# Kernel tuning notes

Measured on AMD Instinct MI355X. Metric: run time of the kernel, lower is better.

The kernel has to match this reference:

```python
import jax, jax.numpy as jnp
import numpy as np

B, S, D, H = 2, 2048, 1024, 16
DH = D // H
EPS = 1e-5
LAMBDA_INIT = 0.8


def setup_inputs() -> dict:
    key = jax.random.key(0)
    ks = jax.random.split(key, 16)
    w_std = 1.0 / np.sqrt(D)
    lam_std = LAMBDA_INIT / np.sqrt(DH)
    return {
        "x": jax.random.normal(ks[0], (B, S, D), jnp.float32),
        # Linear weights stored [in, out] (y = x @ W + b), equivalent to torch W.T
        "Wq": jax.random.normal(ks[1], (D, D), jnp.float32) * w_std,
        "bq": jax.random.normal(ks[2], (D,), jnp.float32) * 0.02,
        "Wk": jax.random.normal(ks[3], (D, D), jnp.float32) * w_std,
        "bk": jax.random.normal(ks[4], (D,), jnp.float32) * 0.02,
        "Wv": jax.random.normal(ks[5], (D, D), jnp.float32) * w_std,
        "bv": jax.random.normal(ks[6], (D,), jnp.float32) * 0.02,
        "Wo": jax.random.normal(ks[7], (D, D), jnp.float32) * w_std,
        "bo": jax.random.normal(ks[8], (D,), jnp.float32) * 0.02,
        "lq1": jax.random.normal(ks[9], (H, DH), jnp.float32) * lam_std,
        "lk1": jax.random.normal(ks[10], (H, DH), jnp.float32) * lam_std,
        "lq2": jax.random.normal(ks[11], (H, DH), jnp.float32) * lam_std,
        "lk2": jax.random.normal(ks[12], (H, DH), jnp.float32) * lam_std,
        # per-head GroupNorm(1, head_dim) affine params (torch default init)
        "gn_w": jnp.ones((H, DH), jnp.float32),
        "gn_b": jnp.zeros((H, DH), jnp.float32),
    }


def reference(x, Wq, bq, Wk, bk, Wv, bv, Wo, bo, lq1, lk1, lq2, lk2, gn_w, gn_b):
    b, s, d = x.shape
    h, dh = lq1.shape
    scale = dh ** -0.5

    q = (x @ Wq + bq).reshape(b, s, h, dh)
    k = (x @ Wk + bk).reshape(b, s, h, dh)
    v = (x @ Wv + bv).reshape(b, s, h, dh)

    # differential lambda per head: exp(<lq1,lk1>) - exp(<lq2,lk2>) + lambda_init
    lam = jnp.exp((lq1 * lk1).sum(-1)) - jnp.exp((lq2 * lk2).sum(-1)) + LAMBDA_INIT  # [H]

    scores = jnp.einsum("bihd,bjhd->bhij", q, k) * scale * lam[None, :, None, None]
    attn = jax.nn.softmax(scores, axis=-1)  # no mask in default call path
    out = jnp.einsum("bhij,bjhd->bihd", attn, v)  # [B,S,H,DH]

    # per-head GroupNorm(1, head_dim): normalize over (seq, head_dim) per (batch, head)
    mean = out.mean(axis=(1, 3), keepdims=True)
    var = out.var(axis=(1, 3), keepdims=True)
    normed = (out - mean) * jax.lax.rsqrt(var + EPS)
    normed = normed * gn_w[None, None, :, :] + gn_b[None, None, :, :]

    y = normed.reshape(b, s, d) @ Wo + bo
    return y
```

## Files before the change

kernel.cpp:

```cpp
#include <hip/hip_runtime.h>

#define S_LEN 2048
#define D_DIM 1024
#define H_NUM 16
#define DH 64
#define EPS_GN 1e-5f
#define LAMBDA_INIT 0.8f

typedef unsigned short bfu;
typedef __attribute__((ext_vector_type(8))) short bf16x8;
typedef __attribute__((ext_vector_type(4))) float f32x4;

union FragU { uint4 u; bf16x8 f; };

__device__ inline float bf2f(bfu u){
  union { unsigned int i; float f; } c; c.i = ((unsigned int)u) << 16; return c.f;
}
__device__ inline bfu f2bf(float f){
  union { float f; unsigned int u; } c; c.f = f;
  unsigned int r = c.u + 0x7fffu + ((c.u >> 16) & 1u);
  return (bfu)(r >> 16);
}
__device__ inline unsigned cvtpk(float lo, float hi){
  unsigned r;
  asm("v_cvt_pk_bf16_f32 %0, %1, %2" : "=v"(r) : "v"(lo), "v"(hi));
  return r;
}
__device__ inline void gload16(const void* g, void* lds){
  __builtin_amdgcn_global_load_lds(
      (const __attribute__((address_space(1))) void*)g,
      (__attribute__((address_space(3))) void*)lds, 16, 0, 0);
}
__device__ inline float ldx(const void* p, size_t i, int isf32){
  return isf32 ? ((const float*)p)[i] : bf2f(((const bfu*)p)[i]);
}
__device__ inline float wave_sum(float x){
  #pragma unroll
  for (int off = 32; off; off >>= 1) x += __shfl_xor(x, off, 64);
  return x;
}

__global__ void lambda_kernel(const void* __restrict__ lq1, const void* __restrict__ lk1,
                              const void* __restrict__ lq2, const void* __restrict__ lk2,
                              const unsigned int* __restrict__ gnw_bits,
                              int* __restrict__ flag, float* __restrict__ lam,
                              float* __restrict__ sums){
  const int isf32 = (gnw_bits[0] == 0x3F800000u) ? 1 : 0;
  int t = threadIdx.x;
  if (t == 0) flag[0] = isf32;
  sums[t] = 0.f;
  if (t < H_NUM){
    float s1 = 0.f, s2 = 0.f;
    for (int d = 0; d < DH; ++d){
      s1 += ldx(lq1, t*DH+d, isf32) * ldx(lk1, t*DH+d, isf32);
      s2 += ldx(lq2, t*DH+d, isf32) * ldx(lk2, t*DH+d, isf32);
    }
    lam[t] = expf(s1) - expf(s2) + LAMBDA_INIT;
  }
}

__global__ __launch_bounds__(256) void prep_all(
    const void* __restrict__ x,
    const void* __restrict__ w0, const void* __restrict__ w1,
    const void* __restrict__ w2, const void* __restrict__ w3,
    const int* __restrict__ flag, bfu* __restrict__ xb, bfu* __restrict__ wt)
{
  const int isf32 = flag[0];
  if (blockIdx.x < 2048){
    size_t i = ((size_t)blockIdx.x * 256 + threadIdx.x) * 8;
    if (isf32){
      const float* xf = (const float*)x;
      float4 a = *(const float4*)(xf + i);
      float4 b = *(const float4*)(xf + i + 4);
      bfu o[8] = {f2bf(a.x),f2bf(a.y),f2bf(a.z),f2bf(a.w),f2bf(b.x),f2bf(b.y),f2bf(b.z),f2bf(b.w)};
      *(uint4*)(xb + i) = *(const uint4*)o;
    } else {
      *(uint4*)(xb + i) = *(const uint4*)((const bfu*)x + i);
    }
    return;
  }
  const int widx = blockIdx.x - 2048;
  const int wsel = widx >> 8, tile = widx & 255;
  const void* W = (wsel==0)?w0:(wsel==1)?w1:(wsel==2)?w2:w3;
  bfu* dst = wt + (size_t)wsel * D_DIM * D_DIM;
  __shared__ float Ts[64][65];
  const int r0 = (tile >> 4) * 64, c0 = (tile & 15) * 64;
  const int ty = threadIdx.x >> 6, tx = threadIdx.x & 63;
  #pragma unroll
  for (int rr = 0; rr < 16; ++rr){
    int row = ty*16 + rr;
    Ts[row][tx] = ldx(W, (size_t)(r0 + row) * D_DIM + c0 + tx, isf32);
  }
  __syncthreads();
  #pragma unroll
  for (int rr = 0; rr < 2; ++rr){
    const int row = rr*32 + (threadIdx.x >> 3);
    const int txg = (threadIdx.x & 7) * 8;
    bfu outv[8];
    #pragma unroll
    for (int k2 = 0; k2 < 8; ++k2) outv[k2] = f2bf(Ts[txg + k2][row]);
    *(uint4*)(dst + (size_t)(c0 + row) * D_DIM + r0 + txg) = *(const uint4*)outv;
  }
}

__global__ __launch_bounds__(256, 3) void qkv_mfma(
    const bfu* __restrict__ xb, const bfu* __restrict__ wt,
    const void* __restrict__ bq, const void* __restrict__ bk, const void* __restrict__ bv,
    const float* __restrict__ lam, const int* __restrict__ flag,
    bfu* __restrict__ qb, bfu* __restrict__ kb, bfu* __restrict__ vt)
{
  const int isf32 = flag[0];
  const int z = blockIdx.z;
  const bfu* Wt = wt + (size_t)z * D_DIM * D_DIM;
  const void* bias = (z==0)?bq:(z==1)?bk:bv;

  __shared__ __align__(16) ushort As[2][128][32];
  __shared__ __align__(16) ushort Bs[2][128][32];
  const int m0 = blockIdx.x * 128, n0 = blockIdx.y * 128;
  const int t = threadIdx.x, w = t >> 6, lane = t & 63;
  const int quad = lane >> 4, l15 = lane & 15;
  const int mbase = (w >> 1) * 64, nbase = (w & 1) * 64;

  const int srow = w*32 + (lane >> 2);
  const int gchunk = (lane & 3) ^ ((lane >> 3) & 3);
  const size_t aoff = (size_t)(m0 + srow) * D_DIM + gchunk*8;
  const size_t boff = (size_t)(n0 + srow) * D_DIM + gchunk*8;

#define STAGE(buf, k0) {                                                  \
    gload16(xb + aoff + (k0),            &As[buf][w*32][0]);              \
    gload16(xb + aoff + 16*D_DIM + (k0), &As[buf][w*32+16][0]);           \
    gload16(Wt + boff + (k0),            &Bs[buf][w*32][0]);              \
    gload16(Wt + boff + 16*D_DIM + (k0), &Bs[buf][w*32+16][0]);           \
  }

  f32x4 acc[4][4];
  #pragma unroll
  for (int i = 0; i < 4; ++i)
    #pragma unroll
    for (int j = 0; j < 4; ++j){ f32x4 zz = {0.f,0.f,0.f,0.f}; acc[i][j] = zz; }

  const int chq = (quad ^ ((l15 >> 1) & 3)) * 8;

  STAGE(0, 0)
  int buf = 0;
  for (int k0 = 0; k0 < D_DIM; k0 += 32){
    if (k0 + 32 < D_DIM){
      STAGE(buf ^ 1, k0 + 32)
      asm volatile("s_waitcnt vmcnt(4)" ::: "memory");
    } else {
      asm volatile("s_waitcnt vmcnt(0)" ::: "memory");
    }
    __builtin_amdgcn_s_barrier();
    FragU af[4], bf[4];
    #pragma unroll
    for (int mt = 0; mt < 4; ++mt) af[mt].u = *(const uint4*)&As[buf][mbase + mt*16 + l15][chq];
    #pragma unroll
    for (int nt = 0; nt < 4; ++nt) bf[nt].u = *(const uint4*)&Bs[buf][nbase + nt*16 + l15][chq];
    #pragma unroll
    for (int mt = 0; mt < 4; ++mt)
      #pragma unroll
      for (int nt = 0; nt < 4; ++nt)
        acc[mt][nt] = __builtin_amdgcn_mfma_f32_16x16x32_bf16(af[mt].f, bf[nt].f, acc[mt][nt], 0, 0, 0);
    __builtin_amdgcn_s_barrier();
    buf ^= 1;
  }
#undef STAGE

  #pragma unroll
  for (int mt = 0; mt < 4; ++mt){
    const int mrow = m0 + mbase + mt*16 + quad*4;
    #pragma unroll
    for (int nt = 0; nt < 4; ++nt){
      const int n = n0 + nbase + nt*16 + l15;
      const float bn = ldx(bias, n, isf32);
      if (z < 2){
        bfu* out = (z == 0) ? qb : kb;
        const float qs = (z == 0) ? 0.18033688f * lam[n >> 6] : 1.0f;
        #pragma unroll
        for (int r = 0; r < 4; ++r)
          out[(size_t)(mrow + r) * D_DIM + n] = f2bf((acc[mt][nt][r] + bn) * qs);
      } else {
        const int b = mrow >> 11, s = mrow & (S_LEN - 1);
        const int h = n >> 6, d = n & 63;
        ushort4 pk;
        pk.x = f2bf(acc[mt][nt][0] + bn); pk.y = f2bf(acc[mt][nt][1] + bn);
        pk.z = f2bf(acc[mt][nt][2] + bn); pk.w = f2bf(acc[mt][nt][3] + bn);
        *(ushort4*)(vt + (((size_t)(b*H_NUM + h)*DH + d)*S_LEN) + s) = pk;
      }
    }
  }
}

__global__ __launch_bounds__(256) void repack_k(const bfu* __restrict__ kb, bfu* __restrict__ ksw){
  __shared__ __align__(16) ushort L[64][72];
  const int b = blockIdx.z, h = blockIdx.y, j0 = blockIdx.x * 64;
  const int t = threadIdx.x;
  const int bh = b*H_NUM + h;
  {
    const int j = t >> 2, seg = (t & 3) * 16;
    const bfu* src = kb + ((size_t)(b*S_LEN + j0 + j)*H_NUM + h)*DH + seg;
    uint4 a = *(const uint4*)src, c = *(const uint4*)(src + 8);
    *(uint4*)&L[j][seg] = a; *(uint4*)&L[j][seg+8] = c;
  }
  __syncthreads();
  #pragma unroll
  for (int half = 0; half < 2; ++half){
    int c16 = half*256 + t;
    int blk = c16 >> 6;
    int l   = c16 & 63;
    int jt = blk >> 1, c = blk & 1;
    int m = l & 15, q = l >> 4;
    uint4 v = *(const uint4*)&L[jt*16 + m][c*32 + q*8];
    bfu* dst = ksw + (((size_t)bh*128 + (j0>>4) + jt)*2 + c)*512 + (size_t)l*8;
    *(uint4*)dst = v;
  }
}

__global__ __launch_bounds__(256) void repack_v(const bfu* __restrict__ vt, bfu* __restrict__ vsw){
  __shared__ __align__(16) ushort L[64][72];
  const int b = blockIdx.z, h = blockIdx.y, j0 = blockIdx.x * 64;
  const int t = threadIdx.x;
  const int bh = b*H_NUM + h;
  {
    const int d = t >> 2, seg = (t & 3) * 16;
    const bfu* src = vt + ((size_t)bh*DH + d)*S_LEN + j0 + seg;
    uint4 a = *(const uint4*)src, c = *(const uint4*)(src + 8);
    *(uint4*)&L[d][seg] = a; *(uint4*)&L[d][seg+8] = c;
  }
  __syncthreads();
  #pragma unroll
  for (int half = 0; half < 2; ++half){
    int c16 = half*256 + t;
    int blk = c16 >> 6;
    int l   = c16 & 63;
    int dt = blk >> 1, jcl = blk & 1;
    int m = l & 15, q = l >> 4;
    const int jb = jcl*32 + 16*(q>>1) + 4*(q&1);
    uint2 v0 = *(const uint2*)&L[dt*16 + m][jb];
    uint2 v1 = *(const uint2*)&L[dt*16 + m][jb + 8];
    uint4 v; v.x = v0.x; v.y = v0.y; v.z = v1.x; v.w = v1.y;
    bfu* dst = vsw + (((size_t)bh*4 + dt)*64 + (j0>>5) + jcl)*512 + (size_t)l*8;
    *(uint4*)dst = v;
  }
}

__global__ __launch_bounds__(256, 2) void attn_mfma(
    const bfu* __restrict__ qb, const bfu* __restrict__ ksw, const bfu* __restrict__ vsw,
    bfu* __restrict__ o, float* __restrict__ sums)
{
  const int wg = blockIdx.x;
  const int swz = (wg & 7) * 64 + (wg >> 3);
  const int g = swz >> 4;
  const int i0 = (swz & 15) * 128;
  const int h = g & 15, b = g >> 4;
  const int t = threadIdx.x, w = t >> 6, lane = t & 63;
  const int quad = lane >> 4, l15 = lane & 15;
  const int bh = g;

  FragU qf[2][2];
  #pragma unroll
  for (int mt = 0; mt < 2; ++mt){
    const bfu* qrow = qb + ((size_t)(b*S_LEN + i0 + w*32 + mt*16 + l15)*H_NUM + h)*DH;
    qf[mt][0].u = *(const uint4*)(qrow + quad*8);
    qf[mt][1].u = *(const uint4*)(qrow + 32 + quad*8);
  }

  const bfu* kbase = ksw + (size_t)bh*131072 + (size_t)lane*8;
  const bfu* vbase = vsw + (size_t)bh*131072 + (size_t)lane*8;

  f32x4 Oacc[2][4];
  #pragma unroll
  for (int mt = 0; mt < 2; ++mt)
    #pragma unroll
    for (int dt = 0; dt < 4; ++dt){ f32x4 zz = {0.f,0.f,0.f,0.f}; Oacc[mt][dt] = zz; }
  f32x4 Lacc[2];
  { f32x4 zz = {0.f,0.f,0.f,0.f}; Lacc[0] = zz; Lacc[1] = zz; }
  FragU ones;
  ones.u.x = ones.u.y = ones.u.z = ones.u.w = 0x3F803F80u;

  FragU kfA[4][2], vfA[2][4], kfB[4][2], vfB[2][4];

#define LOAD_K(KF, J0)                                                          \
  { _Pragma("unroll")                                                           \
    for (int jt = 0; jt < 4; ++jt){                                             \
      const bfu* kr = kbase + (size_t)(((J0)>>4) + jt)*1024;                    \
      KF[jt][0].u = *(const uint4*)kr;                                          \
      KF[jt][1].u = *(const uint4*)(kr + 512);                                  \
    } }
#define LOAD_V(VF, J0)                                                          \
  { _Pragma("unroll")                                                           \
    for (int jt2 = 0; jt2 < 2; ++jt2)                                           \
      _Pragma("unroll")                                                         \
      for (int dt = 0; dt < 4; ++dt)                                            \
        VF[jt2][dt].u = *(const uint4*)(vbase + (size_t)(dt*64 + ((J0)>>5) + jt2)*512); }

#define PIN() { asm volatile("" ::: "memory"); __builtin_amdgcn_sched_barrier(0); }

#define PROCESS(KF, VF)                                                         \
  {                                                                             \
    f32x4 s[2][4];                                                              \
    __builtin_amdgcn_s_setprio(1);                                              \
    _Pragma("unroll")                                                           \
    for (int jt = 0; jt < 4; ++jt){                                             \
      _Pragma("unroll")                                                         \
      for (int mt = 0; mt < 2; ++mt){                                           \
        f32x4 zz = {0.f,0.f,0.f,0.f};                                           \
        zz = __builtin_amdgcn_mfma_f32_16x16x32_bf16(KF[jt][0].f, qf[mt][0].f, zz, 0, 0, 0); \
        zz = __builtin_amdgcn_mfma_f32_16x16x32_bf16(KF[jt][1].f, qf[mt][1].f, zz, 0, 0, 0); \
        s[mt][jt] = zz;                                                         \
      }                                                                         \
    }                                                                           \
    __builtin_amdgcn_s_setprio(0);                                              \
    _Pragma("unroll")                                                           \
    for (int mt = 0; mt < 2; ++mt){                                             \
      _Pragma("unroll")                                                         \
      for (int jt = 0; jt < 4; ++jt){                                           \
        _Pragma("unroll")                                                       \
        for (int r = 0; r < 4; ++r)                                             \
          s[mt][jt][r] = __builtin_exp2f(s[mt][jt][r]);                         \
      }                                                                         \
      _Pragma("unroll")                                                         \
      for (int jt2 = 0; jt2 < 2; ++jt2){                                        \
        unsigned pa0 = cvtpk(s[mt][2*jt2][0],   s[mt][2*jt2][1]);               \
        unsigned pa1 = cvtpk(s[mt][2*jt2][2],   s[mt][2*jt2][3]);               \
        unsigned pb0 = cvtpk(s[mt][2*jt2+1][0], s[mt][2*jt2+1][1]);             \
        unsigned pb1 = cvtpk(s[mt][2*jt2+1][2], s[mt][2*jt2+1][3]);             \
        auto r0 = __builtin_amdgcn_permlane32_swap(pa0, pb0, false, false);     \
        auto r1 = __builtin_amdgcn_permlane32_swap(pa1, pb1, false, false);     \
        FragU pf;                                                               \
        pf.u.x = r0[0]; pf.u.y = r1[0]; pf.u.z = r0[1]; pf.u.w = r1[1];         \
        __builtin_amdgcn_s_setprio(1);                                          \
        _Pragma("unroll")                                                       \
        for (int dt = 0; dt < 4; ++dt)                                          \
          Oacc[mt][dt] = __builtin_amdgcn_mfma_f32_16x16x32_bf16(VF[jt2][dt].f, pf.f, Oacc[mt][dt], 0, 0, 0); \
        Lacc[mt] = __builtin_amdgcn_mfma_f32_16x16x32_bf16(ones.f, pf.f, Lacc[mt], 0, 0, 0); \
        __builtin_amdgcn_s_setprio(0);                                          \
      }                                                                         \
    }                                                                           \
  }

  LOAD_K(kfA, 0)
  LOAD_V(vfA, 0)
  PIN()
  for (int j0 = 0; j0 < S_LEN; j0 += 128){
    LOAD_K(kfB, j0 + 64)
    LOAD_V(vfB, j0 + 64)
    PIN()
    PROCESS(kfA, vfA)
    if (j0 + 128 < S_LEN){
      LOAD_K(kfA, j0 + 128)
      LOAD_V(vfA, j0 + 128)
      PIN()
    }
    PROCESS(kfB, vfB)
  }
#undef LOAD_K
#undef LOAD_V
#undef PROCESS
#undef PIN

  float s1 = 0.f, s2 = 0.f;
  #pragma unroll
  for (int mt = 0; mt < 2; ++mt){
    const float inv = 1.f / Lacc[mt][0];
    bfu* orow = o + ((size_t)(b*S_LEN + i0 + w*32 + mt*16 + l15)*H_NUM + h)*DH;
    #pragma unroll
    for (int dt = 0; dt < 4; ++dt){
      float v0 = Oacc[mt][dt][0]*inv, v1 = Oacc[mt][dt][1]*inv;
      float v2 = Oacc[mt][dt][2]*inv, v3 = Oacc[mt][dt][3]*inv;
      s1 += (v0+v1) + (v2+v3);
      s2 += (v0*v0+v1*v1) + (v2*v2+v3*v3);
      ushort4 pk;
      pk.x = f2bf(v0); pk.y = f2bf(v1); pk.z = f2bf(v2); pk.w = f2bf(v3);
      *(ushort4*)(orow + dt*16 + quad*4) = pk;
    }
  }
  s1 = wave_sum(s1); s2 = wave_sum(s2);
  __shared__ float r1[4], r2[4];
  if (lane == 0){ r1[w] = s1; r2[w] = s2; }
  __syncthreads();
  if (t == 0){
    atomicAdd(&sums[bh*2+0], r1[0]+r1[1]+r1[2]+r1[3]);
    atomicAdd(&sums[bh*2+1], r2[0]+r2[1]+r2[2]+r2[3]);
  }
}

__global__ __launch_bounds__(256) void gn_fold(
    const bfu* __restrict__ wt,
    const void* __restrict__ bo, const float* __restrict__ sums,
    const void* __restrict__ gnw, const void* __restrict__ gnb,
    const int* __restrict__ flag,
    bfu* __restrict__ wt2, float* __restrict__ beta)
{
  const int isf32 = flag[0];
  const int z = blockIdx.y;
  const int t = threadIdx.x;
  const int n = blockIdx.x*16 + (t >> 4);
  const int seg = t & 15;
  const float invN = 1.f / (float)(S_LEN * DH);
  const float s1 = sums[(z*H_NUM + seg)*2], s2 = sums[(z*H_NUM + seg)*2 + 1];
  const float mu = s1 * invN;
  const float ri = rsqrtf(s2 * invN - mu*mu + EPS_GN);
  const bfu* src = wt + (size_t)n * D_DIM + seg*64;
  bfu* dst = wt2 + (size_t)z * D_DIM * D_DIM + (size_t)n * D_DIM + seg*64;
  float bacc = 0.f;
  #pragma unroll
  for (int i0 = 0; i0 < 64; i0 += 8){
    uint4 wv = *(const uint4*)(src + i0);
    const bfu* wp = (const bfu*)&wv;
    bfu outv[8];
    #pragma unroll
    for (int j = 0; j < 8; ++j){
      const int c = seg*64 + i0 + j;
      const float wq = bf2f(wp[j]);
      const float a = ri * ldx(gnw, c, isf32);
      outv[j] = f2bf(wq * a);
      bacc += (ldx(gnb, c, isf32) - mu * a) * wq;
    }
    *(uint4*)(dst + i0) = *(const uint4*)outv;
  }
  #pragma unroll
  for (int off = 1; off < 16; off <<= 1) bacc += __shfl_xor(bacc, off, 64);
  if (seg == 0) beta[z*D_DIM + n] = bacc + ldx(bo, n, isf32);
}

__global__ __launch_bounds__(256) void oproj_mfma(
    const bfu* __restrict__ ob, const bfu* __restrict__ wt2,
    const float* __restrict__ beta, const int* __restrict__ flag, void* __restrict__ y)
{
  const int isf32 = flag[0];
  __shared__ __align__(16) ushort As[64][40];
  __shared__ __align__(16) ushort Bs[128][40];
  const int m0 = blockIdx.x * 64, n0 = blockIdx.y * 128;
  const int t = threadIdx.x, w = t >> 6, lane = t & 63;
  const int quad = lane >> 4, l15 = lane & 15;
  const int mbase = (w >> 1) * 32, nbase = (w & 1) * 64;
  const int bB = m0 >> 11;
  const bfu* Wt = wt2 + (size_t)bB * D_DIM * D_DIM;
  const float* bet = beta + bB * D_DIM;

  const int arow = t >> 2, aseg = (t & 3) * 8;
  const int brow = t >> 1, bhalf = (t & 1) * 16;

  f32x4 acc[2][4];
  #pragma unroll
  for (int i = 0; i < 2; ++i)
    #pragma unroll
    for (int j = 0; j < 4; ++j){ f32x4 zz = {0.f,0.f,0.f,0.f}; acc[i][j] = zz; }

  for (int k0 = 0; k0 < D_DIM; k0 += 32){
    *(uint4*)&As[arow][aseg] = *(const uint4*)(ob + (size_t)(m0 + arow) * D_DIM + k0 + aseg);
    const bfu* bsrc = Wt + (size_t)(n0 + brow) * D_DIM + k0 + bhalf;
    uint4 b0 = *(const uint4*)bsrc, b1 = *(const uint4*)(bsrc + 8);
    *(uint4*)&Bs[brow][bhalf]     = b0;  *(uint4*)&Bs[brow][bhalf + 8] = b1;
    __syncthreads();
    FragU af[2], bfr[4];
    #pragma unroll
    for (int mt = 0; mt < 2; ++mt) af[mt].u = *(const uint4*)&As[mbase + mt*16 + l15][quad*8];
    #pragma unroll
    for (int nt = 0; nt < 4; ++nt) bfr[nt].u = *(const uint4*)&Bs[nbase + nt*16 + l15][quad*8];
    #pragma unroll
    for (int mt = 0; mt < 2; ++mt)
      #pragma unroll
      for (int nt = 0; nt < 4; ++nt)
        acc[mt][nt] = __builtin_amdgcn_mfma_f32_16x16x32_bf16(af[mt].f, bfr[nt].f, acc[mt][nt], 0, 0, 0);
    __syncthreads();
  }

  #pragma unroll
  for (int mt = 0; mt < 2; ++mt){
    const int mrow = m0 + mbase + mt*16 + quad*4;
    #pragma unroll
    for (int nt = 0; nt < 4; ++nt){
      const int n = n0 + nbase + nt*16 + l15;
      const float bn = bet[n];
      #pragma unroll
      for (int r = 0; r < 4; ++r){
        float val = acc[mt][nt][r] + bn;
        if (isf32) ((float*)y)[(size_t)(mrow + r) * D_DIM + n] = val;
        else       ((bfu*)y)[(size_t)(mrow + r) * D_DIM + n] = f2bf(val);
      }
    }
  }
}

extern "C" void kernel_launch(void* const* d_in, const int* in_sizes, int n_in,
                              void* d_out, int out_size, void* d_ws, size_t ws_size,
                              hipStream_t stream)
{
  const void* x   = d_in[0];
  const void* Wq  = d_in[1];
  const void* bq  = d_in[2];
  const void* Wk  = d_in[3];
  const void* bk  = d_in[4];
  const void* Wv  = d_in[5];
  const void* bv  = d_in[6];
  const void* Wo  = d_in[7];
  const void* bo  = d_in[8];
  const void* lq1 = d_in[9];
  const void* lk1 = d_in[10];
  const void* lq2 = d_in[11];
  const void* lk2 = d_in[12];
  const void* gnw = d_in[13];
  const void* gnb = d_in[14];

  float* ws   = (float*)d_ws;
  int*   flag = (int*)d_ws;
  float* lam  = ws + 16;
  float* sums = ws + 48;

  const size_t MB = 1u << 20;
  char* base = (char*)d_ws + 4096;
  bfu* xb  = (bfu*)(base);
  bfu* wt  = (bfu*)(base + 8*MB);
  bfu* qb  = (bfu*)(base + 16*MB);
  bfu* kb  = (bfu*)(base + 24*MB);
  bfu* vt  = (bfu*)(base + 32*MB);
  bfu* ob  = (bfu*)(base + 40*MB);
  bfu* ksw = xb;
  bfu* vsw = kb;
  bfu* wt2 = vt;
  float* beta = (float*)(base + 36*MB);

  lambda_kernel<<<1, 64, 0, stream>>>(lq1, lk1, lq2, lk2, (const unsigned int*)gnw, flag, lam, sums);
  prep_all<<<3072, 256, 0, stream>>>(x, Wq, Wk, Wv, Wo, flag, xb, wt);
  qkv_mfma<<<dim3(32, 8, 3), 256, 0, stream>>>(xb, wt, bq, bk, bv, lam, flag, qb, kb, vt);
  repack_k<<<dim3(32, 16, 2), 256, 0, stream>>>(kb, ksw);
  repack_v<<<dim3(32, 16, 2), 256, 0, stream>>>(vt, vsw);
  attn_mfma<<<512, 256, 0, stream>>>(qb, ksw, vsw, ob, sums);
  gn_fold<<<dim3(64, 2), 256, 0, stream>>>(wt + (size_t)3*D_DIM*D_DIM, bo, sums, gnw, gnb, flag, wt2, beta);
  oproj_mfma<<<dim3(64, 8), 256, 0, stream>>>(ob, wt2, beta, flag, d_out);
}
```

Baseline: 252.4 us.

## Split attention key range across two wave groups with LDS merge

The attention kernel now launches 512 threads per block: two groups of four waves each cover half of the key sequence for the same 128 query rows. Because the softmax is computed without a running max, the partial O and L accumulators simply add. Group 0 writes its partials to shared memory and group 1 combines them, normalizes and writes the output. This doubles the number of waves working on each query tile to raise occupancy and latency hiding. In exchange it adds a shared-memory reduction and a barrier, and the launch bounds now assume 512 threads with 4 waves per EU, which may tighten the register budget.

```diff
diff --git a/kernel.cpp b/kernel.cpp
--- a/kernel.cpp
+++ b/kernel.cpp
@@ -244,23 +244,29 @@
   }
 }
 
-__global__ __launch_bounds__(256, 2) void attn_mfma(
+__global__ __launch_bounds__(512, 4) void attn_mfma(
     const bfu* __restrict__ qb, const bfu* __restrict__ ksw, const bfu* __restrict__ vsw,
     bfu* __restrict__ o, float* __restrict__ sums)
 {
+  __shared__ float OL[128][68];
+  __shared__ float Ls[4][2][16];
+  __shared__ float r1[4], r2[4];
+
   const int wg = blockIdx.x;
   const int swz = (wg & 7) * 64 + (wg >> 3);
   const int g = swz >> 4;
   const int i0 = (swz & 15) * 128;
   const int h = g & 15, b = g >> 4;
   const int t = threadIdx.x, w = t >> 6, lane = t & 63;
+  const int grp = w >> 2, w4 = w & 3;
   const int quad = lane >> 4, l15 = lane & 15;
   const int bh = g;
+  const int jbase = grp * 1024;
 
   FragU qf[2][2];
   #pragma unroll
   for (int mt = 0; mt < 2; ++mt){
-    const bfu* qrow = qb + ((size_t)(b*S_LEN + i0 + w*32 + mt*16 + l15)*H_NUM + h)*DH;
+    const bfu* qrow = qb + ((size_t)(b*S_LEN + i0 + w4*32 + mt*16 + l15)*H_NUM + h)*DH;
     qf[mt][0].u = *(const uint4*)(qrow + quad*8);
     qf[mt][1].u = *(const uint4*)(qrow + 32 + quad*8);
   }
@@ -326,9 +332,9 @@
         unsigned pb0 = cvtpk(s[mt][2*jt2+1][0], s[mt][2*jt2+1][1]);             \
         unsigned pb1 = cvtpk(s[mt][2*jt2+1][2], s[mt][2*jt2+1][3]);             \
         auto r0 = __builtin_amdgcn_permlane32_swap(pa0, pb0, false, false);     \
-        auto r1 = __builtin_amdgcn_permlane32_swap(pa1, pb1, false, false);     \
+        auto r1v = __builtin_amdgcn_permlane32_swap(pa1, pb1, false, false);    \
         FragU pf;                                                               \
-        pf.u.x = r0[0]; pf.u.y = r1[0]; pf.u.z = r0[1]; pf.u.w = r1[1];         \
+        pf.u.x = r0[0]; pf.u.y = r1v[0]; pf.u.z = r0[1]; pf.u.w = r1v[1];       \
         __builtin_amdgcn_s_setprio(1);                                          \
         _Pragma("unroll")                                                       \
         for (int dt = 0; dt < 4; ++dt)                                          \
@@ -339,15 +345,15 @@
     }                                                                           \
   }
 
-  LOAD_K(kfA, 0)
-  LOAD_V(vfA, 0)
+  LOAD_K(kfA, jbase)
+  LOAD_V(vfA, jbase)
   PIN()
-  for (int j0 = 0; j0 < S_LEN; j0 += 128){
+  for (int j0 = jbase; j0 < jbase + 1024; j0 += 128){
     LOAD_K(kfB, j0 + 64)
     LOAD_V(vfB, j0 + 64)
     PIN()
     PROCESS(kfA, vfA)
-    if (j0 + 128 < S_LEN){
+    if (j0 + 128 < jbase + 1024){
       LOAD_K(kfA, j0 + 128)
       LOAD_V(vfA, j0 + 128)
       PIN()
@@ -359,25 +365,39 @@
 #undef PROCESS
 #undef PIN
 
-  float s1 = 0.f, s2 = 0.f;
-  #pragma unroll
-  for (int mt = 0; mt < 2; ++mt){
-    const float inv = 1.f / Lacc[mt][0];
-    bfu* orow = o + ((size_t)(b*S_LEN + i0 + w*32 + mt*16 + l15)*H_NUM + h)*DH;
-    #pragma unroll
-    for (int dt = 0; dt < 4; ++dt){
-      float v0 = Oacc[mt][dt][0]*inv, v1 = Oacc[mt][dt][1]*inv;
-      float v2 = Oacc[mt][dt][2]*inv, v3 = Oacc[mt][dt][3]*inv;
-      s1 += (v0+v1) + (v2+v3);
-      s2 += (v0*v0+v1*v1) + (v2*v2+v3*v3);
-      ushort4 pk;
-      pk.x = f2bf(v0); pk.y = f2bf(v1); pk.z = f2bf(v2); pk.w = f2bf(v3);
-      *(ushort4*)(orow + dt*16 + quad*4) = pk;
-    }
-  }
-  s1 = wave_sum(s1); s2 = wave_sum(s2);
-  __shared__ float r1[4], r2[4];
-  if (lane == 0){ r1[w] = s1; r2[w] = s2; }
+  if (grp == 0){
+    #pragma unroll
+    for (int mt = 0; mt < 2; ++mt){
+      const int il = w4*32 + mt*16 + l15;
+      #pragma unroll
+      for (int dt = 0; dt < 4; ++dt)
+        *(f32x4*)&OL[il][dt*16 + quad*4] = Oacc[mt][dt];
+      if (quad == 0) Ls[w4][mt][l15] = Lacc[mt][0];
+    }
+  }
+  __syncthreads();
+  if (grp == 1){
+    float s1 = 0.f, s2 = 0.f;
+    #pragma unroll
+    for (int mt = 0; mt < 2; ++mt){
+      const int il = w4*32 + mt*16 + l15;
+      const float inv = 1.f / (Lacc[mt][0] + Ls[w4][mt][l15]);
+      bfu* orow = o + ((size_t)(b*S_LEN + i0 + il)*H_NUM + h)*DH;
+      #pragma unroll
+      for (int dt = 0; dt < 4; ++dt){
+        f32x4 p = *(const f32x4*)&OL[il][dt*16 + quad*4];
+        float v0 = (Oacc[mt][dt][0]+p[0])*inv, v1 = (Oacc[mt][dt][1]+p[1])*inv;
+        float v2 = (Oacc[mt][dt][2]+p[2])*inv, v3 = (Oacc[mt][dt][3]+p[3])*inv;
+        s1 += (v0+v1) + (v2+v3);
+        s2 += (v0*v0+v1*v1) + (v2*v2+v3*v3);
+        ushort4 pk;
+        pk.x = f2bf(v0); pk.y = f2bf(v1); pk.z = f2bf(v2); pk.w = f2bf(v3);
+        *(ushort4*)(orow + dt*16 + quad*4) = pk;
+      }
+    }
+    s1 = wave_sum(s1); s2 = wave_sum(s2);
+    if (lane == 0){ r1[w4] = s1; r2[w4] = s2; }
+  }
   __syncthreads();
   if (t == 0){
     atomicAdd(&sums[bh*2+0], r1[0]+r1[1]+r1[2]+r1[3]);
@@ -527,7 +547,7 @@
   qkv_mfma<<<dim3(32, 8, 3), 256, 0, stream>>>(xb, wt, bq, bk, bv, lam, flag, qb, kb, vt);
   repack_k<<<dim3(32, 16, 2), 256, 0, stream>>>(kb, ksw);
   repack_v<<<dim3(32, 16, 2), 256, 0, stream>>>(vt, vsw);
-  attn_mfma<<<512, 256, 0, stream>>>(qb, ksw, vsw, ob, sums);
+  attn_mfma<<<512, 512, 0, stream>>>(qb, ksw, vsw, ob, sums);
   gn_fold<<<dim3(64, 2), 256, 0, stream>>>(wt + (size_t)3*D_DIM*D_DIM, bo, sums, gnw, gnb, flag, wt2, beta);
   oproj_mfma<<<dim3(64, 8), 256, 0, stream>>>(ob, wt2, beta, flag, d_out);
 }
```

New measurement: 544.9 us. 116% more time.

## Merge K/V repack kernels and double-buffer o-proj GEMM with async LDS loads

Applied to the files above, without the earlier changes.

Fuses repack_k and repack_v into a single launch, using a separate workspace buffer for the swizzled V so that K and V no longer alias. Rewrites the output-projection GEMM to use double-buffered direct global-to-LDS loads with an XOR-swizzled unpadded layout and explicit vmcnt waits, so the next tile's loads overlap the current MFMAs. It also adds an occupancy hint of 2 blocks per CU. This adds reliance on the gload16 helper and hand-tuned waitcnt counts.

```diff
diff --git a/kernel.cpp b/kernel.cpp
--- a/kernel.cpp
+++ b/kernel.cpp
@@ -191,56 +191,56 @@
   }
 }
 
-__global__ __launch_bounds__(256) void repack_k(const bfu* __restrict__ kb, bfu* __restrict__ ksw){
+__global__ __launch_bounds__(256) void repack_kv(
+    const bfu* __restrict__ kb, const bfu* __restrict__ vt,
+    bfu* __restrict__ ksw, bfu* __restrict__ vsw)
+{
   __shared__ __align__(16) ushort L[64][72];
-  const int b = blockIdx.z, h = blockIdx.y, j0 = blockIdx.x * 64;
+  const int b = blockIdx.z, hy = blockIdx.y, j0 = blockIdx.x * 64;
   const int t = threadIdx.x;
-  const int bh = b*H_NUM + h;
-  {
-    const int j = t >> 2, seg = (t & 3) * 16;
-    const bfu* src = kb + ((size_t)(b*S_LEN + j0 + j)*H_NUM + h)*DH + seg;
-    uint4 a = *(const uint4*)src, c = *(const uint4*)(src + 8);
-    *(uint4*)&L[j][seg] = a; *(uint4*)&L[j][seg+8] = c;
-  }
-  __syncthreads();
-  #pragma unroll
-  for (int half = 0; half < 2; ++half){
-    int c16 = half*256 + t;
-    int blk = c16 >> 6;
-    int l   = c16 & 63;
-    int jt = blk >> 1, c = blk & 1;
-    int m = l & 15, q = l >> 4;
-    uint4 v = *(const uint4*)&L[jt*16 + m][c*32 + q*8];
-    bfu* dst = ksw + (((size_t)bh*128 + (j0>>4) + jt)*2 + c)*512 + (size_t)l*8;
-    *(uint4*)dst = v;
-  }
-}
-
-__global__ __launch_bounds__(256) void repack_v(const bfu* __restrict__ vt, bfu* __restrict__ vsw){
-  __shared__ __align__(16) ushort L[64][72];
-  const int b = blockIdx.z, h = blockIdx.y, j0 = blockIdx.x * 64;
-  const int t = threadIdx.x;
-  const int bh = b*H_NUM + h;
-  {
-    const int d = t >> 2, seg = (t & 3) * 16;
-    const bfu* src = vt + ((size_t)bh*DH + d)*S_LEN + j0 + seg;
-    uint4 a = *(const uint4*)src, c = *(const uint4*)(src + 8);
-    *(uint4*)&L[d][seg] = a; *(uint4*)&L[d][seg+8] = c;
-  }
-  __syncthreads();
-  #pragma unroll
-  for (int half = 0; half < 2; ++half){
-    int c16 = half*256 + t;
-    int blk = c16 >> 6;
-    int l   = c16 & 63;
-    int dt = blk >> 1, jcl = blk & 1;
-    int m = l & 15, q = l >> 4;
-    const int jb = jcl*32 + 16*(q>>1) + 4*(q&1);
-    uint2 v0 = *(const uint2*)&L[dt*16 + m][jb];
-    uint2 v1 = *(const uint2*)&L[dt*16 + m][jb + 8];
-    uint4 v; v.x = v0.x; v.y = v0.y; v.z = v1.x; v.w = v1.y;
-    bfu* dst = vsw + (((size_t)bh*4 + dt)*64 + (j0>>5) + jcl)*512 + (size_t)l*8;
-    *(uint4*)dst = v;
+  if (hy < 16){
+    const int h = hy, bh = b*H_NUM + h;
+    {
+      const int j = t >> 2, seg = (t & 3) * 16;
+      const bfu* src = kb + ((size_t)(b*S_LEN + j0 + j)*H_NUM + h)*DH + seg;
+      uint4 a = *(const uint4*)src, c = *(const uint4*)(src + 8);
+      *(uint4*)&L[j][seg] = a; *(uint4*)&L[j][seg+8] = c;
+    }
+    __syncthreads();
+    #pragma unroll
+    for (int half = 0; half < 2; ++half){
+      int c16 = half*256 + t;
+      int blk = c16 >> 6;
+      int l   = c16 & 63;
+      int jt = blk >> 1, c = blk & 1;
+      int m = l & 15, q = l >> 4;
+      uint4 v = *(const uint4*)&L[jt*16 + m][c*32 + q*8];
+      bfu* dst = ksw + (((size_t)bh*128 + (j0>>4) + jt)*2 + c)*512 + (size_t)l*8;
+      *(uint4*)dst = v;
+    }
+  } else {
+    const int h = hy - 16, bh = b*H_NUM + h;
+    {
+      const int d = t >> 2, seg = (t & 3) * 16;
+      const bfu* src = vt + ((size_t)bh*DH + d)*S_LEN + j0 + seg;
+      uint4 a = *(const uint4*)src, c = *(const uint4*)(src + 8);
+      *(uint4*)&L[d][seg] = a; *(uint4*)&L[d][seg+8] = c;
+    }
+    __syncthreads();
+    #pragma unroll
+    for (int half = 0; half < 2; ++half){
+      int c16 = half*256 + t;
+      int blk = c16 >> 6;
+      int l   = c16 & 63;
+      int dt = blk >> 1, jcl = blk & 1;
+      int m = l & 15, q = l >> 4;
+      const int jb = jcl*32 + 16*(q>>1) + 4*(q&1);
+      uint2 v0 = *(const uint2*)&L[dt*16 + m][jb];
+      uint2 v1 = *(const uint2*)&L[dt*16 + m][jb + 8];
+      uint4 v; v.x = v0.x; v.y = v0.y; v.z = v1.x; v.w = v1.y;
+      bfu* dst = vsw + (((size_t)bh*4 + dt)*64 + (j0>>5) + jcl)*512 + (size_t)l*8;
+      *(uint4*)dst = v;
+    }
   }
 }
 
@@ -424,13 +424,13 @@
   if (seg == 0) beta[z*D_DIM + n] = bacc + ldx(bo, n, isf32);
 }
 
-__global__ __launch_bounds__(256) void oproj_mfma(
+__global__ __launch_bounds__(256, 2) void oproj_mfma(
     const bfu* __restrict__ ob, const bfu* __restrict__ wt2,
     const float* __restrict__ beta, const int* __restrict__ flag, void* __restrict__ y)
 {
   const int isf32 = flag[0];
-  __shared__ __align__(16) ushort As[64][40];
-  __shared__ __align__(16) ushort Bs[128][40];
+  __shared__ __align__(16) ushort As[2][64][32];
+  __shared__ __align__(16) ushort Bs[2][128][32];
   const int m0 = blockIdx.x * 64, n0 = blockIdx.y * 128;
   const int t = threadIdx.x, w = t >> 6, lane = t & 63;
   const int quad = lane >> 4, l15 = lane & 15;
@@ -439,8 +439,15 @@
   const bfu* Wt = wt2 + (size_t)bB * D_DIM * D_DIM;
   const float* bet = beta + bB * D_DIM;
 
-  const int arow = t >> 2, aseg = (t & 3) * 8;
-  const int brow = t >> 1, bhalf = (t & 1) * 16;
+  const int gchunk = (lane & 3) ^ ((lane >> 3) & 3);
+  const size_t aoff = (size_t)(m0 + w*16 + (lane >> 2)) * D_DIM + gchunk*8;
+  const size_t boff = (size_t)(n0 + w*32 + (lane >> 2)) * D_DIM + gchunk*8;
+
+#define STAGE(buf, k0) {                                              \
+    gload16(ob + aoff + (k0),            &As[buf][w*16][0]);          \
+    gload16(Wt + boff + (k0),            &Bs[buf][w*32][0]);          \
+    gload16(Wt + boff + 16*D_DIM + (k0), &Bs[buf][w*32+16][0]);       \
+  }
 
   f32x4 acc[2][4];
   #pragma unroll
@@ -448,24 +455,32 @@
     #pragma unroll
     for (int j = 0; j < 4; ++j){ f32x4 zz = {0.f,0.f,0.f,0.f}; acc[i][j] = zz; }
 
+  const int chq = (quad ^ ((l15 >> 1) & 3)) * 8;
+
+  STAGE(0, 0)
+  int buf = 0;
   for (int k0 = 0; k0 < D_DIM; k0 += 32){
-    *(uint4*)&As[arow][aseg] = *(const uint4*)(ob + (size_t)(m0 + arow) * D_DIM + k0 + aseg);
-    const bfu* bsrc = Wt + (size_t)(n0 + brow) * D_DIM + k0 + bhalf;
-    uint4 b0 = *(const uint4*)bsrc, b1 = *(const uint4*)(bsrc + 8);
-    *(uint4*)&Bs[brow][bhalf]     = b0;  *(uint4*)&Bs[brow][bhalf + 8] = b1;
-    __syncthreads();
+    if (k0 + 32 < D_DIM){
+      STAGE(buf ^ 1, k0 + 32)
+      asm volatile("s_waitcnt vmcnt(3)" ::: "memory");
+    } else {
+      asm volatile("s_waitcnt vmcnt(0)" ::: "memory");
+    }
+    __builtin_amdgcn_s_barrier();
     FragU af[2], bfr[4];
     #pragma unroll
-    for (int mt = 0; mt < 2; ++mt) af[mt].u = *(const uint4*)&As[mbase + mt*16 + l15][quad*8];
-    #pragma unroll
-    for (int nt = 0; nt < 4; ++nt) bfr[nt].u = *(const uint4*)&Bs[nbase + nt*16 + l15][quad*8];
+    for (int mt = 0; mt < 2; ++mt) af[mt].u = *(const uint4*)&As[buf][mbase + mt*16 + l15][chq];
+    #pragma unroll
+    for (int nt = 0; nt < 4; ++nt) bfr[nt].u = *(const uint4*)&Bs[buf][nbase + nt*16 + l15][chq];
     #pragma unroll
     for (int mt = 0; mt < 2; ++mt)
       #pragma unroll
       for (int nt = 0; nt < 4; ++nt)
         acc[mt][nt] = __builtin_amdgcn_mfma_f32_16x16x32_bf16(af[mt].f, bfr[nt].f, acc[mt][nt], 0, 0, 0);
-    __syncthreads();
-  }
+    __builtin_amdgcn_s_barrier();
+    buf ^= 1;
+  }
+#undef STAGE
 
   #pragma unroll
   for (int mt = 0; mt < 2; ++mt){
@@ -518,15 +533,16 @@
   bfu* vt  = (bfu*)(base + 32*MB);
   bfu* ob  = (bfu*)(base + 40*MB);
   bfu* ksw = xb;
-  bfu* vsw = kb;
+  bfu* vsw = kb + 4*MB/2;
+  vsw = (bfu*)(base + 44*MB);
+  vsw = (bfu*)(base + 48*MB);
   bfu* wt2 = vt;
   float* beta = (float*)(base + 36*MB);
 
   lambda_kernel<<<1, 64, 0, stream>>>(lq1, lk1, lq2, lk2, (const unsigned int*)gnw, flag, lam, sums);
   prep_all<<<3072, 256, 0, stream>>>(x, Wq, Wk, Wv, Wo, flag, xb, wt);
   qkv_mfma<<<dim3(32, 8, 3), 256, 0, stream>>>(xb, wt, bq, bk, bv, lam, flag, qb, kb, vt);
-  repack_k<<<dim3(32, 16, 2), 256, 0, stream>>>(kb, ksw);
-  repack_v<<<dim3(32, 16, 2), 256, 0, stream>>>(vt, vsw);
+  repack_kv<<<dim3(32, 32, 2), 256, 0, stream>>>(kb, vt, ksw, vsw);
   attn_mfma<<<512, 256, 0, stream>>>(qb, ksw, vsw, ob, sums);
   gn_fold<<<dim3(64, 2), 256, 0, stream>>>(wt + (size_t)3*D_DIM*D_DIM, bo, sums, gnw, gnb, flag, wt2, beta);
   oproj_mfma<<<dim3(64, 8), 256, 0, stream>>>(ob, wt2, beta, flag, d_out);
```

Result: no change. 247.9 us (-1.8%).
